# Kernel tuning notes

Hardware: AMD Instinct MI355X
Metric: run time of the kernel (lower is better)

## Reference

```python
import jax, jax.numpy as jnp
import numpy as np

COS_EPS = 1e-08


def setup_inputs() -> dict:
    key = jax.random.key(0)
    k1, k2, k3, k4, k5 = jax.random.split(key, 5)
    B, N, C = 4, 4096, 128
    q_node = jax.random.normal(k1, (B, N, C), dtype=jnp.float32)
    k_node = jax.random.normal(k2, (B, N, C), dtype=jnp.float32)
    v_node = jax.random.normal(k3, (B, N, C), dtype=jnp.float32)
    # shared Linear(h_dim, h_dim): torch default init scale ~ 1/sqrt(C)
    W = jax.random.normal(k4, (C, C), dtype=jnp.float32) / jnp.sqrt(jnp.float32(C))
    b = jax.random.normal(k5, (C,), dtype=jnp.float32) / jnp.sqrt(jnp.float32(C))
    return {"q_node": q_node, "k_node": k_node, "v_node": v_node, "W": W, "b": b}


def reference(q_node, k_node, v_node, W, b):
    # shared projection applied to q, k, v
    q = jnp.einsum('bnc,cd->bnd', q_node, W.T) + b
    k = jnp.einsum('bnc,cd->bnd', k_node, W.T) + b
    v = jnp.einsum('bnc,cd->bnd', v_node, W.T) + b
    # cosine similarity scores: [B, Nq, Nk]
    qn = jnp.linalg.norm(q, axis=2, keepdims=True)        # [B, Nq, 1]
    kn = jnp.linalg.norm(k, axis=2, keepdims=True)        # [B, Nk, 1]
    scores = jnp.einsum('bqc,bkc->bqk', q, k)
    cos_sim = scores / (qn * jnp.swapaxes(kn, 1, 2) + COS_EPS)
    # sum-normalization (not softmax)
    edge_weight = cos_sim / (cos_sim.sum(axis=2, keepdims=True) + 1e-08)
    # weighted aggregation: [B, Nq, C]
    return jnp.einsum('bqk,bkc->bqc', edge_weight, v)
```

## Files before the change

### kernel.cpp

```cpp
#include <hip/hip_runtime.h>

#define BB 4
#define NN 4096
#define CC 128
#define NROWS (BB * NN)

#define QN_OFF  0
#define QP_OFF  (QN_OFF + NROWS)
#define MM_OFF  (QP_OFF + NROWS * CC)
#define KS_OFF  (MM_OFF + BB * CC * CC)
#define PP_OFF  (KS_OFF + BB * CC)
#define KP_OFF  (PP_OFF + 256 * CC * CC)

typedef __attribute__((ext_vector_type(8))) short short8;
typedef __attribute__((ext_vector_type(4))) float f32x4;

__device__ __forceinline__ void fma4(float4& a, const float4 x,
    const float4 w0, const float4 w1, const float4 w2, const float4 w3)
{
    a.x += x.x * w0.x + x.y * w1.x + x.z * w2.x + x.w * w3.x;
    a.y += x.x * w0.y + x.y * w1.y + x.z * w2.y + x.w * w3.y;
    a.z += x.x * w0.z + x.y * w1.z + x.z * w2.z + x.w * w3.z;
    a.w += x.x * w0.w + x.y * w1.w + x.z * w2.w + x.w * w3.w;
}

__device__ __forceinline__ float dot4(const float4 x, const float4 k)
{
    return x.x * k.x + x.y * k.y + x.z * k.z + x.w * k.w;
}

__device__ __forceinline__ unsigned short f2bf(float f)
{
    union { float f; unsigned u; } v; v.f = f;
    unsigned r = (v.u + 0x7fffu + ((v.u >> 16) & 1u)) >> 16;
    return (unsigned short)r;
}
__device__ __forceinline__ float bf2f(unsigned short h)
{
    union { unsigned u; float f; } v; v.u = ((unsigned)h) << 16;
    return v.f;
}

__global__ __launch_bounds__(512, 1) void projpb_kernel(
    const float* __restrict__ q_node, const float* __restrict__ k_node,
    const float* __restrict__ v_node, const float* __restrict__ W,
    const float* __restrict__ bias, float* __restrict__ ws)
{
    __shared__ __align__(16) unsigned short Wsp[3 * CC * CC];
    __shared__ float4 red[512];
    unsigned short* Whi = Wsp;
    unsigned short* Wmd = Wsp + CC * CC;
    unsigned short* Wlo = Wsp + 2 * CC * CC;

    const int tid = threadIdx.x;

    for (int e = tid; e < CC * CC; e += 512) {
        int col = e >> 7, k = e & 127;
        float wv = W[e];
        unsigned short hi = f2bf(wv);
        float r1 = wv - bf2f(hi);
        unsigned short md = f2bf(r1);
        unsigned short lo = f2bf(r1 - bf2f(md));
        int idx = (col << 7) + ((((k >> 3) ^ (col & 7)) << 3) | (k & 7));
        Whi[idx] = hi; Wmd[idx] = md; Wlo[idx] = lo;
    }

    const int blk  = blockIdx.x;
    const int base = blk * 64;
    const int w    = tid >> 6;
    const int lane = tid & 63;
    const int l15  = lane & 15;
    const int lg   = lane >> 4;
    const bool isq = (w < 4);
    const int rt   = w & 3;
    const float* X = isq ? q_node : k_node;
    const int arow = base + rt * 16 + l15;

    f32x4 acc[8];
#pragma unroll
    for (int ct = 0; ct < 8; ct++) {
        float b = bias[ct * 16 + l15];
        acc[ct] = (f32x4){b, b, b, b};
    }

    __syncthreads();

    const float* Xr = X + (size_t)arow * CC;
#pragma unroll
    for (int ks = 0; ks < 4; ks++) {
        const int k0 = ks * 32 + lg * 8;
        float4 xa = *(const float4*)(Xr + k0);
        float4 xb = *(const float4*)(Xr + k0 + 4);
        float xs[8] = {xa.x, xa.y, xa.z, xa.w, xb.x, xb.y, xb.z, xb.w};
        short8 Ahi, Amd, Alo;
#pragma unroll
        for (int j = 0; j < 8; j++) {
            unsigned short h = f2bf(xs[j]);
            float r1 = xs[j] - bf2f(h);
            unsigned short m = f2bf(r1);
            Ahi[j] = (short)h;
            Amd[j] = (short)m;
            Alo[j] = (short)f2bf(r1 - bf2f(m));
        }
        const int slot = ks * 4 + lg;
#pragma unroll
        for (int ct = 0; ct < 8; ct++) {
            int col  = ct * 16 + l15;
            int fidx = (col << 7) + ((slot ^ (col & 7)) << 3);
            short8 Bhi = *(const short8*)(Whi + fidx);
            short8 Bmd = *(const short8*)(Wmd + fidx);
            short8 Blo = *(const short8*)(Wlo + fidx);
            acc[ct] = __builtin_amdgcn_mfma_f32_16x16x32_bf16(Ahi, Bhi, acc[ct], 0, 0, 0);
            acc[ct] = __builtin_amdgcn_mfma_f32_16x16x32_bf16(Ahi, Bmd, acc[ct], 0, 0, 0);
            acc[ct] = __builtin_amdgcn_mfma_f32_16x16x32_bf16(Amd, Bhi, acc[ct], 0, 0, 0);
            acc[ct] = __builtin_amdgcn_mfma_f32_16x16x32_bf16(Ahi, Blo, acc[ct], 0, 0, 0);
            acc[ct] = __builtin_amdgcn_mfma_f32_16x16x32_bf16(Amd, Bmd, acc[ct], 0, 0, 0);
            acc[ct] = __builtin_amdgcn_mfma_f32_16x16x32_bf16(Alo, Bhi, acc[ct], 0, 0, 0);
        }
    }

    float ss[4];
#pragma unroll
    for (int r = 0; r < 4; r++) {
        float t = 0.f;
#pragma unroll
        for (int ct = 0; ct < 8; ct++) t += acc[ct][r] * acc[ct][r];
#pragma unroll
        for (int off = 8; off > 0; off >>= 1) t += __shfl_xor(t, off, 16);
        ss[r] = t;
    }

    if (isq) {
#pragma unroll
        for (int r = 0; r < 4; r++) {
            int gr = base + rt * 16 + lg * 4 + r;
            float* qp = ws + QP_OFF + (size_t)gr * CC;
#pragma unroll
            for (int ct = 0; ct < 8; ct++) qp[ct * 16 + l15] = acc[ct][r];
            if (l15 == 0) ws[QN_OFF + gr] = sqrtf(ss[r]);
        }
    }

    __syncthreads();

    float* Khs = (float*)Wsp;
    float* Vs  = Khs + 8192;

    if (!isq) {
#pragma unroll
        for (int r = 0; r < 4; r++) {
            float inv = 1.0f / sqrtf(ss[r]);
            int lr = rt * 16 + lg * 4 + r;
            float* kp = Khs + lr * CC;
#pragma unroll
            for (int ct = 0; ct < 8; ct++) kp[ct * 16 + l15] = acc[ct][r] * inv;
        }
    }

    const int c4v = tid & 31, nrv = tid >> 5;
    const float* Vp = v_node + (size_t)base * CC;
#pragma unroll
    for (int i = 0; i < 4; i++) {
        int n = nrv + i * 16;
        ((float4*)(Vs + n * CC))[c4v] = ((const float4*)(Vp + (size_t)n * CC))[c4v];
    }
    __syncthreads();

    float4 ksum4 = make_float4(0.f, 0.f, 0.f, 0.f);
#pragma unroll
    for (int i = 0; i < 4; i++) {
        int n = nrv + i * 16;
        float4 kv = ((const float4*)(Khs + n * CC))[c4v];
        ksum4.x += kv.x; ksum4.y += kv.y; ksum4.z += kv.z; ksum4.w += kv.w;
    }

    const int dg2 = tid & 15, cg = tid >> 4;
    float a2[4][8];
#pragma unroll
    for (int i = 0; i < 4; i++)
#pragma unroll
        for (int j = 0; j < 8; j++) a2[i][j] = 0.f;

#define P2L(ka, va, vb, n)                                  \
    ka = *(const float4*)(Khs + (n) * CC + 4 * cg);         \
    va = *(const float4*)(Vs + (n) * CC + 4 * dg2);         \
    vb = *(const float4*)(Vs + (n) * CC + 64 + 4 * dg2);
#define P2F(ka, va, vb)                                     \
    {  float kc[4] = {ka.x, ka.y, ka.z, ka.w};              \
       float vd[8] = {va.x, va.y, va.z, va.w,               \
                      vb.x, vb.y, vb.z, vb.w};              \
       _Pragma("unroll")                                    \
       for (int i = 0; i < 4; i++)                          \
           { _Pragma("unroll")                              \
             for (int j = 0; j < 8; j++)                    \
                 a2[i][j] += kc[i] * vd[j]; } }

    {
        float4 kaA, vaA, vbA, kaB, vaB, vbB;
        P2L(kaA, vaA, vbA, 0)
        for (int n = 0; n <= 60; n += 2) {
            P2L(kaB, vaB, vbB, n + 1)
            P2F(kaA, vaA, vbA)
            P2L(kaA, vaA, vbA, n + 2)
            P2F(kaB, vaB, vbB)
        }
        P2L(kaB, vaB, vbB, 63)
        P2F(kaA, vaA, vbA)
        P2F(kaB, vaB, vbB)
    }
#undef P2L
#undef P2F

    float* pp = ws + PP_OFF + (size_t)blk * (CC * CC);
#pragma unroll
    for (int i = 0; i < 4; i++) {
        int c = 4 * cg + i;
        *(float4*)(pp + c * CC + 4 * dg2) =
            make_float4(a2[i][0], a2[i][1], a2[i][2], a2[i][3]);
        *(float4*)(pp + c * CC + 64 + 4 * dg2) =
            make_float4(a2[i][4], a2[i][5], a2[i][6], a2[i][7]);
    }

    red[nrv * 32 + c4v] = ksum4;
    __syncthreads();
    if (tid < 32) {
        float4 sm = red[tid];
#pragma unroll
        for (int i = 1; i < 16; i++) {
            float4 t = red[i * 32 + tid];
            sm.x += t.x; sm.y += t.y; sm.z += t.z; sm.w += t.w;
        }
        ((float4*)(ws + KP_OFF + (size_t)blk * CC))[tid] = sm;
    }
}

__global__ __launch_bounds__(256) void mchain_kernel(const float* __restrict__ W,
                                                     const float* __restrict__ bias,
                                                     float* __restrict__ ws)
{
    __shared__ float4 W4s[CC * 32];
    __shared__ float4 m0q[4][2][32];
    __shared__ float m0row[2][CC];
    __shared__ float kpart[4];
    __shared__ float ksl[2];
    const int tid = threadIdx.x;
    const int b = blockIdx.y, x = blockIdx.x;
    const int c0 = x * 2;

    for (int idx = tid; idx < CC * 32; idx += 256) {
        int e = idx >> 5, d4 = idx & 31;
        W4s[(e << 5) + (d4 ^ (e & 31))] = ((const float4*)W)[idx];
    }

    {
        const int q  = tid >> 6;
        const int r  = (tid >> 5) & 1;
        const int c4 = tid & 31;
        const float4* pp = (const float4*)(ws + PP_OFF
                         + (size_t)(b * 64 + q * 16) * (CC * CC)
                         + (size_t)(c0 + r) * CC) + c4;
        float4 s0 = make_float4(0.f, 0.f, 0.f, 0.f);
#pragma unroll 4
        for (int p = 0; p < 16; p++) {
            float4 t = pp[(size_t)p * (CC * CC / 4)];
            s0.x += t.x; s0.y += t.y; s0.z += t.z; s0.w += t.w;
        }
        m0q[q][r][c4] = s0;
    }

    {
        const int rr = tid >> 7, p = tid & 127;
        float v = 0.f;
        if (p < 64) v = ws[KP_OFF + (size_t)(b * 64 + p) * CC + c0 + rr];
#pragma unroll
        for (int off = 32; off > 0; off >>= 1) v += __shfl_xor(v, off, 64);
        if ((tid & 63) == 0) kpart[tid >> 6] = v;
    }
    __syncthreads();

    if (tid < 64) {
        const int r = tid >> 5, c4 = tid & 31;
        float4 a = m0q[0][r][c4], bq = m0q[1][r][c4];
        float4 c = m0q[2][r][c4], d = m0q[3][r][c4];
        float4 s;
        s.x = (a.x + bq.x) + (c.x + d.x);
        s.y = (a.y + bq.y) + (c.y + d.y);
        s.z = (a.z + bq.z) + (c.z + d.z);
        s.w = (a.w + bq.w) + (c.w + d.w);
        ((float4*)&m0row[r][0])[c4] = s;
    }
    if (tid < 2) {
        float s = kpart[tid * 2] + kpart[tid * 2 + 1];
        ksl[tid] = s;
        ws[KS_OFF + b * CC + c0 + tid] = s;
    }
    __syncthreads();

    const int r = tid >> 7, e = tid & 127;
    const float4* mr = (const float4*)m0row[r];
    float m = 0.f;
#pragma unroll
    for (int d4 = 0; d4 < 32; d4++) {
        float4 a4 = mr[d4];
        float4 w4 = W4s[(e << 5) + (d4 ^ (e & 31))];
        m += a4.x * w4.x + a4.y * w4.y + a4.z * w4.z + a4.w * w4.w;
    }
    m += ksl[r] * bias[e];
    ws[MM_OFF + (size_t)b * CC * CC + (size_t)(c0 + r) * CC + e] = m;
}

__global__ __launch_bounds__(512, 2) void out_kernel(const float* __restrict__ ws,
                                                     float* __restrict__ out)
{
    __shared__ float Ml[CC * CC];

    const int blk = blockIdx.x;
    const int b = blk >> 6;
    const int r0 = (blk & 63) * 64;
    const float* M = ws + MM_OFF + (size_t)b * CC * CC;
    const int tid = threadIdx.x;

    for (int e = tid; e < CC * CC / 4; e += 512)
        ((float4*)Ml)[e] = ((const float4*)M)[e];

    const float4* Ks4 = (const float4*)(ws + KS_OFF + b * CC);
    const int dg = tid & 31, rg = tid >> 5;
    const int row = r0 + rg * 4;
    const float4* Qv = (const float4*)(ws + QP_OFF + ((size_t)b * NN + row) * CC);
    const float4* Mv = (const float4*)Ml;

    float4 acc[4];
    float s[4];
#pragma unroll
    for (int i = 0; i < 4; i++) {
        acc[i] = make_float4(0.f, 0.f, 0.f, 0.f);
        s[i] = 0.f;
    }

    __syncthreads();

#define OLW(m0, m1, m2, m3, ks, c)               \
    m0 = Mv[(((c) + 0) << 5) + dg];              \
    m1 = Mv[(((c) + 1) << 5) + dg];              \
    m2 = Mv[(((c) + 2) << 5) + dg];              \
    m3 = Mv[(((c) + 3) << 5) + dg];              \
    ks = Ks4[(c) >> 2];
#define OLX(xv, c)                                 \
    { const int c4_ = (c) >> 2;                    \
      xv[0] = Qv[c4_];      xv[1] = Qv[32 + c4_];  \
      xv[2] = Qv[64 + c4_]; xv[3] = Qv[96 + c4_]; }
#define OFM(m0, m1, m2, m3, ks, xv)                  \
    _Pragma("unroll")                                \
    for (int i_ = 0; i_ < 4; i_++) {                 \
        fma4(acc[i_], xv[i_], m0, m1, m2, m3);       \
        s[i_] += dot4(xv[i_], ks);                   \
    }

    {
        float4 mA0, mA1, mA2, mA3, mB0, mB1, mB2, mB3;
        float4 ksA, ksB, xA[4], xB[4];
        OLW(mA0, mA1, mA2, mA3, ksA, 0)
        OLX(xA, 0)
        for (int c = 0; c <= CC - 16; c += 8) {
            OLW(mB0, mB1, mB2, mB3, ksB, c + 4)
            OLX(xB, c + 4)
            OFM(mA0, mA1, mA2, mA3, ksA, xA)
            OLW(mA0, mA1, mA2, mA3, ksA, c + 8)
            OLX(xA, c + 8)
            OFM(mB0, mB1, mB2, mB3, ksB, xB)
        }
        OLW(mB0, mB1, mB2, mB3, ksB, CC - 4)
        OLX(xB, CC - 4)
        OFM(mA0, mA1, mA2, mA3, ksA, xA)
        OFM(mB0, mB1, mB2, mB3, ksB, xB)
    }
#undef OLW
#undef OLX
#undef OFM

    float* op = out + ((size_t)b * NN + row) * CC;
    const float* qn = ws + QN_OFF + (size_t)b * NN + row;
#pragma unroll
    for (int i = 0; i < 4; i++) {
        float inv = 1.0f / (s[i] + 1e-8f * qn[i]);
        float4 o = acc[i];
        o.x *= inv; o.y *= inv; o.z *= inv; o.w *= inv;
        ((float4*)(op + (size_t)i * CC))[dg] = o;
    }
}

extern "C" void kernel_launch(void* const* d_in, const int* in_sizes, int n_in,
                              void* d_out, int out_size, void* d_ws, size_t ws_size,
                              hipStream_t stream)
{
    const float* q_node = (const float*)d_in[0];
    const float* k_node = (const float*)d_in[1];
    const float* v_node = (const float*)d_in[2];
    const float* W      = (const float*)d_in[3];
    const float* bias   = (const float*)d_in[4];
    float* out = (float*)d_out;
    float* ws  = (float*)d_ws;

    projpb_kernel<<<256, 512, 0, stream>>>(q_node, k_node, v_node, W, bias, ws);
    mchain_kernel<<<dim3(64, BB), 256, 0, stream>>>(W, bias, ws);
    out_kernel<<<256, 512, 0, stream>>>(ws, out);
}
```

Before: 121.3 us.

## Compute output GEMM with bf16x3 split MFMA instead of scalar FP32 FMAs

Replaces the scalar float4 FMA loop in out_kernel with MFMA 16x16x32 bf16 instructions. Both operands are split into hi/mid/lo bf16 parts and six cross products are accumulated to approximate FP32 accuracy. M is stored in shared memory as three swizzled bf16 planes, and the row sum for normalization is computed separately and reduced across lanes. This moves the compute to the matrix cores at the cost of per-element splitting work, 6x MFMA count, lower occupancy (launch bounds 1) and uncoalesced scalar output stores.

```diff
diff --git a/kernel.cpp b/kernel.cpp
--- a/kernel.cpp
+++ b/kernel.cpp
@@ -14,15 +14,6 @@
 
 typedef __attribute__((ext_vector_type(8))) short short8;
 typedef __attribute__((ext_vector_type(4))) float f32x4;
-
-__device__ __forceinline__ void fma4(float4& a, const float4 x,
-    const float4 w0, const float4 w1, const float4 w2, const float4 w3)
-{
-    a.x += x.x * w0.x + x.y * w1.x + x.z * w2.x + x.w * w3.x;
-    a.y += x.x * w0.y + x.y * w1.y + x.z * w2.y + x.w * w3.y;
-    a.z += x.x * w0.z + x.y * w1.z + x.z * w2.z + x.w * w3.z;
-    a.w += x.x * w0.w + x.y * w1.w + x.z * w2.w + x.w * w3.w;
-}
 
 __device__ __forceinline__ float dot4(const float4 x, const float4 k)
 {
@@ -309,83 +300,98 @@
     ws[MM_OFF + (size_t)b * CC * CC + (size_t)(c0 + r) * CC + e] = m;
 }
 
-__global__ __launch_bounds__(512, 2) void out_kernel(const float* __restrict__ ws,
+__global__ __launch_bounds__(512, 1) void out_kernel(const float* __restrict__ ws,
                                                      float* __restrict__ out)
 {
-    __shared__ float Ml[CC * CC];
-
+    __shared__ __align__(16) unsigned short Msp[3 * CC * CC];
+    __shared__ float Ksl[CC];
+    unsigned short* Mhi = Msp;
+    unsigned short* Mmd = Msp + CC * CC;
+    unsigned short* Mlo = Msp + 2 * CC * CC;
+
+    const int tid = threadIdx.x;
     const int blk = blockIdx.x;
-    const int b = blk >> 6;
+    const int b  = blk >> 6;
     const int r0 = (blk & 63) * 64;
     const float* M = ws + MM_OFF + (size_t)b * CC * CC;
-    const int tid = threadIdx.x;
-
-    for (int e = tid; e < CC * CC / 4; e += 512)
-        ((float4*)Ml)[e] = ((const float4*)M)[e];
-
-    const float4* Ks4 = (const float4*)(ws + KS_OFF + b * CC);
-    const int dg = tid & 31, rg = tid >> 5;
-    const int row = r0 + rg * 4;
-    const float4* Qv = (const float4*)(ws + QP_OFF + ((size_t)b * NN + row) * CC);
-    const float4* Mv = (const float4*)Ml;
-
-    float4 acc[4];
-    float s[4];
-#pragma unroll
-    for (int i = 0; i < 4; i++) {
-        acc[i] = make_float4(0.f, 0.f, 0.f, 0.f);
-        s[i] = 0.f;
-    }
-
-    __syncthreads();
-
-#define OLW(m0, m1, m2, m3, ks, c)               \
-    m0 = Mv[(((c) + 0) << 5) + dg];              \
-    m1 = Mv[(((c) + 1) << 5) + dg];              \
-    m2 = Mv[(((c) + 2) << 5) + dg];              \
-    m3 = Mv[(((c) + 3) << 5) + dg];              \
-    ks = Ks4[(c) >> 2];
-#define OLX(xv, c)                                 \
-    { const int c4_ = (c) >> 2;                    \
-      xv[0] = Qv[c4_];      xv[1] = Qv[32 + c4_];  \
-      xv[2] = Qv[64 + c4_]; xv[3] = Qv[96 + c4_]; }
-#define OFM(m0, m1, m2, m3, ks, xv)                  \
-    _Pragma("unroll")                                \
-    for (int i_ = 0; i_ < 4; i_++) {                 \
-        fma4(acc[i_], xv[i_], m0, m1, m2, m3);       \
-        s[i_] += dot4(xv[i_], ks);                   \
-    }
-
-    {
-        float4 mA0, mA1, mA2, mA3, mB0, mB1, mB2, mB3;
-        float4 ksA, ksB, xA[4], xB[4];
-        OLW(mA0, mA1, mA2, mA3, ksA, 0)
-        OLX(xA, 0)
-        for (int c = 0; c <= CC - 16; c += 8) {
-            OLW(mB0, mB1, mB2, mB3, ksB, c + 4)
-            OLX(xB, c + 4)
-            OFM(mA0, mA1, mA2, mA3, ksA, xA)
-            OLW(mA0, mA1, mA2, mA3, ksA, c + 8)
-            OLX(xA, c + 8)
-            OFM(mB0, mB1, mB2, mB3, ksB, xB)
-        }
-        OLW(mB0, mB1, mB2, mB3, ksB, CC - 4)
-        OLX(xB, CC - 4)
-        OFM(mA0, mA1, mA2, mA3, ksA, xA)
-        OFM(mB0, mB1, mB2, mB3, ksB, xB)
-    }
-#undef OLW
-#undef OLX
-#undef OFM
-
-    float* op = out + ((size_t)b * NN + row) * CC;
-    const float* qn = ws + QN_OFF + (size_t)b * NN + row;
-#pragma unroll
-    for (int i = 0; i < 4; i++) {
-        float inv = 1.0f / (s[i] + 1e-8f * qn[i]);
-        float4 o = acc[i];
-        o.x *= inv; o.y *= inv; o.z *= inv; o.w *= inv;
-        ((float4*)(op + (size_t)i * CC))[dg] = o;
+
+    for (int e = tid; e < CC * CC; e += 512) {
+        int k = e >> 7, col = e & 127;
+        float mv = M[e];
+        unsigned short hi = f2bf(mv);
+        float r1 = mv - bf2f(hi);
+        unsigned short md = f2bf(r1);
+        unsigned short lo = f2bf(r1 - bf2f(md));
+        int idx = (col << 7) + ((((k >> 3) ^ (col & 7)) << 3) | (k & 7));
+        Mhi[idx] = hi; Mmd[idx] = md; Mlo[idx] = lo;
+    }
+    if (tid < CC) Ksl[tid] = ws[KS_OFF + b * CC + tid];
+
+    const int w    = tid >> 6;
+    const int lane = tid & 63;
+    const int l15  = lane & 15;
+    const int lg   = lane >> 4;
+    const int rt   = w & 3;
+    const int ch   = w >> 2;
+
+    const int arow = r0 + rt * 16 + l15;
+    const float* Xr = ws + QP_OFF + ((size_t)b * NN + arow) * CC;
+
+    f32x4 acc[4];
+#pragma unroll
+    for (int ct = 0; ct < 4; ct++) acc[ct] = (f32x4){0.f, 0.f, 0.f, 0.f};
+    float sp = 0.f;
+
+    __syncthreads();
+
+#pragma unroll
+    for (int ks = 0; ks < 4; ks++) {
+        const int k0 = ks * 32 + lg * 8;
+        float4 xa = *(const float4*)(Xr + k0);
+        float4 xb = *(const float4*)(Xr + k0 + 4);
+        float xs[8] = {xa.x, xa.y, xa.z, xa.w, xb.x, xb.y, xb.z, xb.w};
+        short8 Ahi, Amd, Alo;
+#pragma unroll
+        for (int j = 0; j < 8; j++) {
+            unsigned short h = f2bf(xs[j]);
+            float r1 = xs[j] - bf2f(h);
+            unsigned short m = f2bf(r1);
+            Ahi[j] = (short)h;
+            Amd[j] = (short)m;
+            Alo[j] = (short)f2bf(r1 - bf2f(m));
+            sp += xs[j] * Ksl[k0 + j];
+        }
+        const int slot = ks * 4 + lg;
+#pragma unroll
+        for (int ct = 0; ct < 4; ct++) {
+            int col  = ch * 64 + ct * 16 + l15;
+            int fidx = (col << 7) + ((slot ^ (col & 7)) << 3);
+            short8 Bhi = *(const short8*)(Mhi + fidx);
+            short8 Bmd = *(const short8*)(Mmd + fidx);
+            short8 Blo = *(const short8*)(Mlo + fidx);
+            acc[ct] = __builtin_amdgcn_mfma_f32_16x16x32_bf16(Ahi, Bhi, acc[ct], 0, 0, 0);
+            acc[ct] = __builtin_amdgcn_mfma_f32_16x16x32_bf16(Ahi, Bmd, acc[ct], 0, 0, 0);
+            acc[ct] = __builtin_amdgcn_mfma_f32_16x16x32_bf16(Amd, Bhi, acc[ct], 0, 0, 0);
+            acc[ct] = __builtin_amdgcn_mfma_f32_16x16x32_bf16(Ahi, Blo, acc[ct], 0, 0, 0);
+            acc[ct] = __builtin_amdgcn_mfma_f32_16x16x32_bf16(Amd, Bmd, acc[ct], 0, 0, 0);
+            acc[ct] = __builtin_amdgcn_mfma_f32_16x16x32_bf16(Alo, Bhi, acc[ct], 0, 0, 0);
+        }
+    }
+
+    sp += __shfl_xor(sp, 16, 64);
+    sp += __shfl_xor(sp, 32, 64);
+
+#pragma unroll
+    for (int r = 0; r < 4; r++) {
+        const int rowt = lg * 4 + r;
+        float srow = __shfl(sp, rowt, 64);
+        const int gr = r0 + rt * 16 + rowt;
+        float qn = ws[QN_OFF + (size_t)b * NN + gr];
+        float inv = 1.0f / (srow + 1e-8f * qn);
+        float* op = out + ((size_t)b * NN + gr) * CC + ch * 64;
+#pragma unroll
+        for (int ct = 0; ct < 4; ct++)
+            op[ct * 16 + l15] = acc[ct][r] * inv;
     }
 }
 
```

Measured after the change: 122.0 us. Within noise of the previous version (+0.6%).
